# Kernel tuning notes

Measured on AMD Instinct MI355X. Metric: run time of the kernel, lower is better.

Reference implementation:

```python
import jax, jax.numpy as jnp
import numpy as np


def setup_inputs() -> dict:
    key = jax.random.key(0)
    k1, k2 = jax.random.split(key)
    N, C, H, W = 4, 32, 512, 512
    gH, gW = 512, 512
    x = jax.random.normal(k1, (N, C, H, W), dtype=jnp.float32)
    # pixel-space sampling coords: xgrid in [0, W-1), ygrid in [0, H-1)
    grid = jax.random.uniform(k2, (N, gH, gW, 2), dtype=jnp.float32)
    grid = grid * jnp.array([W - 1.0, H - 1.0], dtype=jnp.float32)
    return {"x": x, "grid": grid}


def reference(x, grid):
    # x: [N, C, H, W], grid: [N, gH, gW, 2] (pixel coords)
    N, C, H, W = x.shape
    gH, gW = grid.shape[1], grid.shape[2]
    xg = grid[..., 0:1]  # [N, gH, gW, 1]
    yg = grid[..., 1:2]
    mask = ((xg >= 0) & (yg >= 0) & (xg < W - 1) & (yg < H - 1)).astype(x.dtype)
    x0f = jnp.floor(xg)
    x1f = x0f + 1.0
    y0f = jnp.floor(yg)
    y1f = y0f + 1.0
    # bilinear weights, shape [1, N, gH, gW] (matches torch .permute(3,0,1,2))
    wa = ((x1f - xg) * (y1f - yg)).transpose(3, 0, 1, 2)
    wb = ((x1f - xg) * (yg - y0f)).transpose(3, 0, 1, 2)
    wc = ((xg - x0f) * (y1f - yg)).transpose(3, 0, 1, 2)
    wd = ((xg - x0f) * (yg - y0f)).transpose(3, 0, 1, 2)
    # masked integer corner indices, [N, gH, gW]
    x0 = (x0f * mask).reshape(N, gH, gW).astype(jnp.int32)
    y0 = (y0f * mask).reshape(N, gH, gW).astype(jnp.int32)
    x1 = (x1f * mask).reshape(N, gH, gW).astype(jnp.int32)
    y1 = (y1f * mask).reshape(N, gH, gW).astype(jnp.int32)
    ind = jnp.broadcast_to(jnp.arange(N)[:, None, None], (N, gH, gW))
    xp = x.transpose(1, 0, 2, 3)  # [C, N, H, W]
    # 4 corner gathers -> [C, N, gH, gW], weighted sum, back to [N, C, gH, gW]
    out = (xp[:, ind, y0, x0] * wa
           + xp[:, ind, y1, x0] * wb
           + xp[:, ind, y0, x1] * wc
           + xp[:, ind, y1, x1] * wd).transpose(1, 0, 2, 3)
    return out * mask.transpose(0, 3, 1, 2)  # mask broadcasts over C
```

## Files before the change

### kernel.cpp

```cpp
#include <hip/hip_runtime.h>


#define N_  4
#define C_  32
#define H_  512
#define W_  512
#define HW_ (H_ * W_)
#define GHW_ (512 * 512)
#define QT_ 256

typedef unsigned int u32x4 __attribute__((ext_vector_type(4)));

__device__ __forceinline__ float bf16u_to_f32(unsigned int u16) {
    return __uint_as_float(u16 << 16);
}

__device__ __forceinline__ void quant_one(const float* v, unsigned int* qw,
                                          unsigned short* sbits) {
    float mx = 0.0f;
    #pragma unroll
    for (int c = 0; c < C_; ++c) mx = fmaxf(mx, fabsf(v[c]));

    unsigned short sb = 0;
    float inv = 0.0f;
    if (mx > 0.0f) {
        const float s0 = mx * (1.0f / 127.0f);
        const unsigned int ub = (__float_as_uint(s0) + 0xFFFFu) >> 16;
        sb = (unsigned short)ub;
        inv = 1.0f / bf16u_to_f32(ub);
    }
    #pragma unroll
    for (int w = 0; w < 8; ++w) {
        unsigned int word = 0;
        #pragma unroll
        for (int b = 0; b < 4; ++b) {
            int qi = __float2int_rn(v[4 * w + b] * inv) + 127;
            qi = min(max(qi, 0), 254);
            word |= ((unsigned int)qi) << (8 * b);
        }
        qw[w] = word;
    }
    *sbits = sb;
}

__global__ __launch_bounds__(256) void quant_pack_v6(
    const float* __restrict__ x,
    unsigned int* __restrict__ q2,
    unsigned int* __restrict__ sc2)
{
    __shared__ unsigned int   qw[QT_ + 1][8];
    __shared__ unsigned short sh[QT_ + 1];

    const int n   = blockIdx.x >> 10;
    const int hw0 = (blockIdx.x & 1023) << 8;
    const int j   = threadIdx.x;
    const int hw  = hw0 + j;

    float v[C_];
    const float* xp = x + (size_t)n * (C_ * HW_) + hw;
    #pragma unroll
    for (int c = 0; c < C_; ++c)
        v[c] = __builtin_nontemporal_load(xp + (size_t)c * HW_);

    quant_one(v, qw[j], &sh[j]);

    if (j == 255) {
        int hwn = hw + 1;
        if (hwn >= HW_) hwn = hw;
        const float* xq = x + (size_t)n * (C_ * HW_) + hwn;
        float v2[C_];
        #pragma unroll
        for (int c = 0; c < C_; ++c)
            v2[c] = __builtin_nontemporal_load(xq + (size_t)c * HW_);
        quant_one(v2, qw[256], &sh[256]);
    }
    __syncthreads();

    const int y  = hw0 >> 9;
    const int xb = hw0 & 511;
    const size_t g0 = (size_t)n * HW_ +
                      ((size_t)(y >> 1) << 10) + ((size_t)xb << 1) + (y & 1);

    u32x4* dst = (u32x4*)q2;
    #pragma unroll
    for (int r = 0; r < 4; ++r) {
        const int s    = r * 256 + j;
        const int k    = s >> 2;
        const int part = s & 3;
        const unsigned int* src = (part < 2) ? qw[k] : qw[k + 1];
        const int o = (part & 1) * 4;
        u32x4 val = {src[o], src[o + 1], src[o + 2], src[o + 3]};
        __builtin_nontemporal_store(val, dst + (g0 + 2 * (size_t)k) * 4 + part);
    }
    sc2[(size_t)n * HW_ + hw] =
        (unsigned int)sh[j] | ((unsigned int)sh[j + 1] << 16);
}

__global__ __launch_bounds__(256) void grid_sample_q8i(
    const uint4* __restrict__ q2,
    const unsigned int* __restrict__ sc2,
    const float* __restrict__ gridp,
    float* __restrict__ out)
{
    const int t  = blockIdx.x * blockDim.x + threadIdx.x;
    const int n  = t >> 18;
    const int ij = t & 0x3FFFF;

    const float2 gv = reinterpret_cast<const float2*>(gridp)[t];
    const float xg = gv.x;
    const float yg = gv.y;

    const bool m = (xg >= 0.0f) & (yg >= 0.0f) &
                   (xg < (float)(W_ - 1)) & (yg < (float)(H_ - 1));

    float* o = out + (size_t)n * (C_ * GHW_) + ij;

    if (!m) {
        #pragma unroll
        for (int c = 0; c < C_; ++c) o[c * GHW_] = 0.0f;
        return;
    }

    const float x0f = floorf(xg);
    const float y0f = floorf(yg);
    const int   x0  = (int)x0f;
    const int   y0  = (int)y0f;
    const float fx  = xg - x0f;
    const float fy  = yg - y0f;
    const float wa = (1.0f - fx) * (1.0f - fy);
    const float wb = (1.0f - fx) * fy;
    const float wc = fx * (1.0f - fy);
    const float wd = fx * fy;

    const size_t img = (size_t)n * HW_;

    const size_t g0 = img + ((size_t)(y0 >> 1) << 10) + ((size_t)x0 << 1) + (y0 & 1);
    const size_t g1 = (y0 & 1)
        ? img + (((size_t)(y0 >> 1) + 1) << 10) + ((size_t)x0 << 1)
        : g0 + 1;
    const uint4* p0 = q2 + g0 * 4;
    const uint4* p1 = q2 + g1 * 4;

    const uint4 r0a = p0[0], r0b = p0[1], r0c = p0[2], r0d = p0[3];
    const uint4 r1a = p1[0], r1b = p1[1], r1c = p1[2], r1d = p1[3];

    const size_t tb = img + (size_t)(y0 * W_ + x0);
    const unsigned int s0 = sc2[tb];
    const unsigned int s1 = sc2[tb + W_];

    const float sA = bf16u_to_f32(s0 & 0xFFFFu);
    const float sC = bf16u_to_f32(s0 >> 16);
    const float sB = bf16u_to_f32(s1 & 0xFFFFu);
    const float sD = bf16u_to_f32(s1 >> 16);

    const float WA = wa * sA, WB = wb * sB, WC = wc * sC, WD = wd * sD;
    const float K  = 127.0f * (WA + WB + WC + WD);

    const unsigned int q00[8] = {r0a.x, r0a.y, r0a.z, r0a.w, r0b.x, r0b.y, r0b.z, r0b.w};
    const unsigned int q01[8] = {r0c.x, r0c.y, r0c.z, r0c.w, r0d.x, r0d.y, r0d.z, r0d.w};
    const unsigned int q10[8] = {r1a.x, r1a.y, r1a.z, r1a.w, r1b.x, r1b.y, r1b.z, r1b.w};
    const unsigned int q11[8] = {r1c.x, r1c.y, r1c.z, r1c.w, r1d.x, r1d.y, r1d.z, r1d.w};

    float acc[C_];
    #pragma unroll
    for (int w = 0; w < 8; ++w) {
        const unsigned int a = q00[w], b = q10[w], c = q01[w], d = q11[w];
        #pragma unroll
        for (int bb = 0; bb < 4; ++bb) {
            const int sh = 8 * bb;
            const float fa = (float)((a >> sh) & 0xFFu);
            const float fb = (float)((b >> sh) & 0xFFu);
            const float fc = (float)((c >> sh) & 0xFFu);
            const float fd = (float)((d >> sh) & 0xFFu);
            acc[4 * w + bb] = WA * fa + WB * fb + WC * fc + WD * fd - K;
        }
    }

    #pragma unroll
    for (int c = 0; c < C_; ++c) o[c * GHW_] = acc[c];
}

__global__ __launch_bounds__(256) void grid_sample_nchw(
    const float* __restrict__ x,
    const float* __restrict__ gridp,
    float* __restrict__ out)
{
    const int t  = blockIdx.x * blockDim.x + threadIdx.x;
    const int n  = t >> 18;
    const int ij = t & 0x3FFFF;
    const float2 gv = reinterpret_cast<const float2*>(gridp)[t];
    const float xg = gv.x, yg = gv.y;
    const bool m = (xg >= 0.0f) & (yg >= 0.0f) &
                   (xg < (float)(W_ - 1)) & (yg < (float)(H_ - 1));
    float* o = out + (size_t)n * (C_ * GHW_) + ij;
    if (!m) {
        #pragma unroll
        for (int c = 0; c < C_; ++c) o[c * GHW_] = 0.0f;
        return;
    }
    const float x0f = floorf(xg), y0f = floorf(yg);
    const int x0 = (int)x0f, y0 = (int)y0f;
    const float fx = xg - x0f, fy = yg - y0f;
    const float wa = (1.0f - fx) * (1.0f - fy);
    const float wb = (1.0f - fx) * fy;
    const float wc = fx * (1.0f - fy);
    const float wd = fx * fy;
    const float* xp = x + (size_t)n * (C_ * HW_) + y0 * W_ + x0;
    #pragma unroll
    for (int c = 0; c < C_; ++c) {
        const float* p = xp + c * HW_;
        o[c * GHW_] = wa * p[0] + wb * p[W_] + wc * p[1] + wd * p[W_ + 1];
    }
}

extern "C" void kernel_launch(void* const* d_in, const int* in_sizes, int n_in,
                              void* d_out, int out_size, void* d_ws, size_t ws_size,
                              hipStream_t stream) {
    const float* x     = (const float*)d_in[0];
    const float* gridp = (const float*)d_in[1];
    float* out         = (float*)d_out;

    const size_t q2_bytes  = (size_t)N_ * HW_ * 64;
    const size_t sc2_bytes = (size_t)N_ * HW_ * sizeof(unsigned);

    if (ws_size >= q2_bytes + sc2_bytes) {
        unsigned int* q2  = (unsigned int*)d_ws;
        unsigned int* sc2 = (unsigned int*)((char*)d_ws + q2_bytes);
        quant_pack_v6<<<N_ * 1024, 256, 0, stream>>>(x, q2, sc2);
        grid_sample_q8i<<<N_ * 1024, 256, 0, stream>>>(
            (const uint4*)q2, sc2, gridp, out);
    } else {
        grid_sample_nchw<<<(N_ * GHW_) / 256, 256, 0, stream>>>(x, gridp, out);
    }
}
```

Baseline: 126.1 us.

## Interleave per-batch quantize and sample launches, retune temporal store hints

Instead of quantizing all four batch images and then sampling all of them, the host now runs the quantize kernel and the sampling kernel once per batch image. The packed int8 image a sampler reads was just written, so it is more likely still in cache. The packed-image stores become normal cached stores, and the large float output stores become nontemporal so they do not evict the packed data. The cost is more kernel launches and smaller grids per launch, with less parallelism for each kernel.

```diff
diff --git a/kernel.cpp b/kernel.cpp
--- a/kernel.cpp
+++ b/kernel.cpp
@@ -9,8 +9,6 @@
 #define GHW_ (512 * 512)
 #define QT_ 256
 
-typedef unsigned int u32x4 __attribute__((ext_vector_type(4)));
-
 __device__ __forceinline__ float bf16u_to_f32(unsigned int u16) {
     return __uint_as_float(u16 << 16);
 }
@@ -43,16 +41,16 @@
     *sbits = sb;
 }
 
-__global__ __launch_bounds__(256) void quant_pack_v6(
+__global__ __launch_bounds__(256) void quant_pack_v7(
     const float* __restrict__ x,
     unsigned int* __restrict__ q2,
-    unsigned int* __restrict__ sc2)
+    unsigned int* __restrict__ sc2,
+    int n)
 {
     __shared__ unsigned int   qw[QT_ + 1][8];
     __shared__ unsigned short sh[QT_ + 1];
 
-    const int n   = blockIdx.x >> 10;
-    const int hw0 = (blockIdx.x & 1023) << 8;
+    const int hw0 = blockIdx.x << 8;
     const int j   = threadIdx.x;
     const int hw  = hw0 + j;
 
@@ -81,7 +79,7 @@
     const size_t g0 = (size_t)n * HW_ +
                       ((size_t)(y >> 1) << 10) + ((size_t)xb << 1) + (y & 1);
 
-    u32x4* dst = (u32x4*)q2;
+    uint4* dst = (uint4*)q2;
     #pragma unroll
     for (int r = 0; r < 4; ++r) {
         const int s    = r * 256 + j;
@@ -89,22 +87,22 @@
         const int part = s & 3;
         const unsigned int* src = (part < 2) ? qw[k] : qw[k + 1];
         const int o = (part & 1) * 4;
-        u32x4 val = {src[o], src[o + 1], src[o + 2], src[o + 3]};
-        __builtin_nontemporal_store(val, dst + (g0 + 2 * (size_t)k) * 4 + part);
+        dst[(g0 + 2 * (size_t)k) * 4 + part] =
+            make_uint4(src[o], src[o + 1], src[o + 2], src[o + 3]);
     }
     sc2[(size_t)n * HW_ + hw] =
         (unsigned int)sh[j] | ((unsigned int)sh[j + 1] << 16);
 }
 
-__global__ __launch_bounds__(256) void grid_sample_q8i(
+__global__ __launch_bounds__(256) void grid_sample_q8v7(
     const uint4* __restrict__ q2,
     const unsigned int* __restrict__ sc2,
     const float* __restrict__ gridp,
-    float* __restrict__ out)
+    float* __restrict__ out,
+    int n)
 {
-    const int t  = blockIdx.x * blockDim.x + threadIdx.x;
-    const int n  = t >> 18;
-    const int ij = t & 0x3FFFF;
+    const int ij = blockIdx.x * blockDim.x + threadIdx.x;
+    const int t  = (n << 18) + ij;
 
     const float2 gv = reinterpret_cast<const float2*>(gridp)[t];
     const float xg = gv.x;
@@ -117,7 +115,8 @@
 
     if (!m) {
         #pragma unroll
-        for (int c = 0; c < C_; ++c) o[c * GHW_] = 0.0f;
+        for (int c = 0; c < C_; ++c)
+            __builtin_nontemporal_store(0.0f, o + c * GHW_);
         return;
     }
 
@@ -177,7 +176,8 @@
     }
 
     #pragma unroll
-    for (int c = 0; c < C_; ++c) o[c * GHW_] = acc[c];
+    for (int c = 0; c < C_; ++c)
+        __builtin_nontemporal_store(acc[c], o + c * GHW_);
 }
 
 __global__ __launch_bounds__(256) void grid_sample_nchw(
@@ -226,9 +226,11 @@
     if (ws_size >= q2_bytes + sc2_bytes) {
         unsigned int* q2  = (unsigned int*)d_ws;
         unsigned int* sc2 = (unsigned int*)((char*)d_ws + q2_bytes);
-        quant_pack_v6<<<N_ * 1024, 256, 0, stream>>>(x, q2, sc2);
-        grid_sample_q8i<<<N_ * 1024, 256, 0, stream>>>(
-            (const uint4*)q2, sc2, gridp, out);
+        for (int n = 0; n < N_; ++n) {
+            quant_pack_v7<<<HW_ / QT_, 256, 0, stream>>>(x, q2, sc2, n);
+            grid_sample_q8v7<<<GHW_ / 256, 256, 0, stream>>>(
+                (const uint4*)q2, sc2, gridp, out, n);
+        }
     } else {
         grid_sample_nchw<<<(N_ * GHW_) / 256, 256, 0, stream>>>(x, gridp, out);
     }
```

Result: no change. 124.8 us (-1.0%).
